# Kernel optimization log

Hardware: AMD Instinct MI355X
Metric: run time of the kernel (lower is better)

## Reference

```python
import jax, jax.numpy as jnp
import numpy as np

B, T, K = 16, 8, 4          # batch, num task vectors, num param blocks
DIN, H1, F, MH = 9408, 1024, 512, 128  # encoder dims; MetaNet hidden


def _pool(x):
    # 4x4 average pool then flatten: [B,3,224,224] -> [B, 3*56*56]
    b = x.shape[0]
    return x.reshape(b, 3, 56, 4, 56, 4).mean(axis=(3, 5)).reshape(b, -1)


def setup_inputs() -> dict:
    key = jax.random.key(0)
    ks = jax.random.split(key, 13)
    n = lambda k, shp, sc: jax.random.normal(k, shp, jnp.float32) * sc
    return {
        "x": jax.random.normal(ks[0], (B, 3, 224, 224), jnp.float32),
        "W1": n(ks[1], (DIN, H1), 0.02), "b1": n(ks[2], (H1,), 0.02),
        "W2": n(ks[3], (H1, F), 0.02),  "b2": n(ks[4], (F,), 0.02),
        "dW1": n(ks[5], (T, DIN, H1), 0.01), "db1": n(ks[6], (T, H1), 0.01),
        "dW2": n(ks[7], (T, H1, F), 0.01),   "db2": n(ks[8], (T, F), 0.01),
        # MetaNet: Linear(F,MH) init std=0.01, ReLU, Linear(MH, T*K)
        "mW1": n(ks[9], (F, MH), 0.01), "mb1": n(ks[10], (MH,), 0.01),
        "mW2": n(ks[11], (MH, T * K), 0.02), "mb2": n(ks[12], (T * K,), 0.02),
    }


def reference(x, W1, b1, W2, b2, dW1, db1, dW2, db2, mW1, mb1, mW2, mb2):
    xp = _pool(x)  # [B, DIN]
    # base features with frozen base params (torch.no_grad)
    base = jax.lax.stop_gradient(
        jax.nn.relu(xp @ W1 + b1) @ W2 + b2)  # [B, F]
    # MetaNet -> blockwise coefficients [B, T, K]; block order (W1,b1,W2,b2)
    coefs = (jax.nn.relu(base @ mW1 + mb1) @ mW2 + mb2).reshape(B, T, K)
    cW1, cb1, cW2, cb2 = coefs[:, :, 0], coefs[:, :, 1], coefs[:, :, 2], coefs[:, :, 3]
    # per-sample composed forward; (W1 + sum_t c*dW1) applied to xp, factored
    # so the [B,DIN,H1] composed weight is never materialized:
    h_tv = jnp.einsum("bi,tij->btj", xp, dW1)            # [B,T,H1]
    h = jax.nn.relu(xp @ W1 + jnp.einsum("bt,btj->bj", cW1, h_tv)
                    + b1 + jnp.einsum("bt,tj->bj", cb1, db1))  # [B,H1]
    o_tv = jnp.einsum("bj,tjk->btk", h, dW2)             # [B,T,F]
    out = (h @ W2 + jnp.einsum("bt,btk->bk", cW2, o_tv)
           + b2 + jnp.einsum("bt,tk->bk", cb2, db2))     # [B,F]
    return out
```

## Files before the change

### kernel.cpp

```cpp
#include <hip/hip_runtime.h>
#include <cstdint>
#include <cstddef>


typedef float f2_t __attribute__((ext_vector_type(2)));
typedef float f4_t __attribute__((ext_vector_type(4)));

template<int KC, int VEC, int UF, int NT>
__device__ __forceinline__ void gemm_pipe(
    const float* a_s, int row0, const float* Brow, int N, float (&acc)[16][VEC])
{
  static_assert(KC % UF == 0, "");
  constexpr int NG = KC / UF;
  static_assert(NG >= 2, "");
  float w0[UF][VEC], w1[UF][VEC];

  auto loadg = [&](float (&W)[UF][VEC], int kb) {
#pragma unroll
    for (int u = 0; u < UF; ++u) {
      const float* p = Brow + (size_t)(kb + u) * N;
      if constexpr (VEC == 2) {
        f2_t v;
        if constexpr (NT) v = __builtin_nontemporal_load(reinterpret_cast<const f2_t*>(p));
        else              v = *reinterpret_cast<const f2_t*>(p);
        W[u][0] = v.x; W[u][1] = v.y;
      } else {
        f4_t v;
        if constexpr (NT) v = __builtin_nontemporal_load(reinterpret_cast<const f4_t*>(p));
        else              v = *reinterpret_cast<const f4_t*>(p);
        W[u][0] = v.x; W[u][1] = v.y; W[u][2] = v.z; W[u][3] = v.w;
      }
    }
  };
  auto comp = [&](const float (&W)[UF][VEC], int kb) {
#pragma unroll
    for (int u = 0; u < UF; ++u) {
      int kk = row0 + kb + u;
      const float4 a0 = *reinterpret_cast<const float4*>(&a_s[kk * 20 + 0]);
      const float4 a1 = *reinterpret_cast<const float4*>(&a_s[kk * 20 + 4]);
      const float4 a2 = *reinterpret_cast<const float4*>(&a_s[kk * 20 + 8]);
      const float4 a3 = *reinterpret_cast<const float4*>(&a_s[kk * 20 + 12]);
      const float av[16] = {a0.x, a0.y, a0.z, a0.w, a1.x, a1.y, a1.z, a1.w,
                            a2.x, a2.y, a2.z, a2.w, a3.x, a3.y, a3.z, a3.w};
#pragma unroll
      for (int b = 0; b < 16; ++b)
#pragma unroll
        for (int v = 0; v < VEC; ++v)
          acc[b][v] = fmaf(av[b], W[u][v], acc[b][v]);
    }
  };

  loadg(w0, 0);
  if constexpr (NG % 2 == 0) {
#pragma unroll 1
    for (int g = 0; g + 2 < NG; g += 2) {
      loadg(w1, (g + 1) * UF);
      comp(w0, g * UF);
      loadg(w0, (g + 2) * UF);
      comp(w1, (g + 1) * UF);
    }
    loadg(w1, (NG - 1) * UF);
    comp(w0, (NG - 2) * UF);
    comp(w1, (NG - 1) * UF);
  } else {
#pragma unroll 1
    for (int g = 0; g + 3 < NG; g += 2) {
      loadg(w1, (g + 1) * UF);
      comp(w0, g * UF);
      loadg(w0, (g + 2) * UF);
      comp(w1, (g + 1) * UF);
    }
    loadg(w1, (NG - 2) * UF);
    comp(w0, (NG - 3) * UF);
    loadg(w0, (NG - 1) * UF);
    comp(w1, (NG - 2) * UF);
    comp(w0, (NG - 1) * UF);
  }
}

template<int KC, int NTHR>
__device__ __forceinline__ void stage_pool(float* a_s, const float* __restrict__ x, int il) {
  for (int idx = threadIdx.x; idx < 16 * KC; idx += NTHR) {
    int b = idx / KC, kk = idx - b * KC;
    int i = il + kk;
    int ch = i / 3136, r = i - ch * 3136;
    int pi = r / 56, pj = r - pi * 56;
    const float* src = x + ((size_t)(b * 3 + ch) * 224 + 4 * pi) * 224 + 4 * pj;
    float4 v0 = *reinterpret_cast<const float4*>(src);
    float4 v1 = *reinterpret_cast<const float4*>(src + 224);
    float4 v2 = *reinterpret_cast<const float4*>(src + 448);
    float4 v3 = *reinterpret_cast<const float4*>(src + 672);
    float s = (v0.x + v0.y + v0.z + v0.w) + (v1.x + v1.y + v1.z + v1.w)
            + (v2.x + v2.y + v2.z + v2.w) + (v3.x + v3.y + v3.z + v3.w);
    a_s[kk * 20 + b] = s * 0.0625f;
  }
}

__global__ __launch_bounds__(512, 2) void gbig_kernel(
    const float* __restrict__ x,
    const float* __restrict__ W1,
    const float* __restrict__ dW1,
    float* __restrict__ P1, float* __restrict__ P3)
{
  __shared__ float a_s[294 * 20];
  __shared__ float lds2[256 * 65];
  const int tid = threadIdx.x;

  if (blockIdx.x < 112) {
    const int c = blockIdx.x;
    stage_pool<84, 512>(a_s, x, c * 84);
    __syncthreads();

    const int j0 = tid * 2;
    float acc[16][2];
#pragma unroll
    for (int b = 0; b < 16; ++b) { acc[b][0] = 0.f; acc[b][1] = 0.f; }
    gemm_pipe<84, 2, 7, 1>(a_s, 0, W1 + (size_t)c * 84 * 1024 + j0, 1024, acc);

    float* Pb = P1 + (size_t)c * 16 * 1024 + j0;
#pragma unroll
    for (int b = 0; b < 16; ++b) {
      f2_t v = {acc[b][0], acc[b][1]};
      __builtin_nontemporal_store(v, reinterpret_cast<f2_t*>(Pb));
      Pb += 1024;
    }
  } else {
    const int c = blockIdx.x - 112;
    const int t = c >> 5, il = (c & 31) * 294;
    stage_pool<294, 512>(a_s, x, il);
    __syncthreads();

    const int half = tid >> 8, t256 = tid & 255;
    const int j0 = t256 * 4;
    float acc[16][4];
#pragma unroll
    for (int b = 0; b < 16; ++b)
#pragma unroll
      for (int v = 0; v < 4; ++v) acc[b][v] = 0.f;

    gemm_pipe<147, 4, 7, 1>(a_s, half * 147,
                            dW1 + ((size_t)t * 9408 + il + half * 147) * 1024 + j0,
                            1024, acc);

    if (half) {
      float* dst = &lds2[t256 * 65];
#pragma unroll
      for (int b = 0; b < 16; ++b)
#pragma unroll
        for (int v = 0; v < 4; ++v) dst[b * 4 + v] = acc[b][v];
    }
    __syncthreads();
    if (!half) {
      const float* src = &lds2[t256 * 65];
      float* Pb = P3 + (size_t)c * 16 * 1024 + j0;
#pragma unroll
      for (int b = 0; b < 16; ++b) {
        f4_t v = {acc[b][0] + src[b * 4 + 0], acc[b][1] + src[b * 4 + 1],
                  acc[b][2] + src[b * 4 + 2], acc[b][3] + src[b * 4 + 3]};
        __builtin_nontemporal_store(v, reinterpret_cast<f4_t*>(Pb));
        Pb += 1024;
      }
    }
  }
}

__global__ __launch_bounds__(256) void rg12_kernel(
    const float* __restrict__ P1, const float* __restrict__ b1,
    const float* __restrict__ W2,
    float* __restrict__ z1, float* __restrict__ P2)
{
  __shared__ float4 r[16][17];
  __shared__ float t1s[64];
  const int blk = blockIdx.x;
  const int b = blk >> 4, jg = blk & 15;
  const int fl = threadIdx.x & 15, s = threadIdx.x >> 4;
  const int f = blk * 64 + fl * 4;

  const f4_t* p = reinterpret_cast<const f4_t*>(P1 + (size_t)s * 7 * 16384 + f);
  float sx = 0.f, sy = 0.f, sz = 0.f, sw = 0.f;
#pragma unroll
  for (int cc = 0; cc < 7; ++cc) {
    f4_t v = __builtin_nontemporal_load(p);
    sx += v.x; sy += v.y; sz += v.z; sw += v.w;
    p += 4096;
  }
  r[s][fl] = make_float4(sx, sy, sz, sw);
  __syncthreads();

  if (s == 0) {
    float vx = 0.f, vy = 0.f, vz = 0.f, vw = 0.f;
#pragma unroll
    for (int i = 0; i < 16; ++i) {
      float4 t = r[i][fl];
      vx += t.x; vy += t.y; vz += t.z; vw += t.w;
    }
    float4 bb = *reinterpret_cast<const float4*>(b1 + (f & 1023));
    float4 z = make_float4(vx + bb.x, vy + bb.y, vz + bb.z, vw + bb.w);
    *reinterpret_cast<float4*>(z1 + f) = z;
    *reinterpret_cast<float4*>(&t1s[fl * 4]) =
        make_float4(fmaxf(z.x, 0.f), fmaxf(z.y, 0.f), fmaxf(z.z, 0.f), fmaxf(z.w, 0.f));
  }
  __syncthreads();

  const int j = threadIdx.x * 2;
  const float* w = W2 + (size_t)(jg * 64) * 512 + j;
  float a0 = 0.f, a1 = 0.f;
#pragma unroll 8
  for (int kk = 0; kk < 64; ++kk) {
    f2_t wv = *reinterpret_cast<const f2_t*>(w);
    w += 512;
    float tv = t1s[kk];
    a0 = fmaf(tv, wv.x, a0);
    a1 = fmaf(tv, wv.y, a1);
  }
  f2_t o = {a0, a1};
  __builtin_nontemporal_store(o, reinterpret_cast<f2_t*>(P2 + ((size_t)jg * 16 + b) * 512 + j));
}

template<int KC, int VEC, int UF, int NT, int BS>
__global__ __launch_bounds__(BS) void skinny_gemm(
    const float* __restrict__ A, int ldA,
    const float* __restrict__ B,
    const float* __restrict__ A2, int ldA2,
    const float* __restrict__ B2,
    int chunkSplit, int chunksPerT,
    const float* __restrict__ coefs4,
    int N, float* __restrict__ P)
{
  __shared__ float a_s[KC * 20];
  const int c = blockIdx.x, tid = threadIdx.x;

  const float* Ab;
  const float* Bb;
  int lda, iLoc0, t = 0;
  bool scaled = false;
  if (c < chunkSplit) {
    Ab = A; lda = ldA;
    if (chunksPerT > 0) {
      t = c / chunksPerT;
      iLoc0 = (c - t * chunksPerT) * KC;
    } else {
      iLoc0 = c * KC;
    }
    scaled = (coefs4 != nullptr);
    Bb = B + (size_t)c * KC * N;
  } else {
    Ab = A2; lda = ldA2;
    iLoc0 = (c - chunkSplit) * KC;
    Bb = B2 + (size_t)iLoc0 * N;
  }

  for (int b = 0; b < 16; ++b) {
    float s = scaled ? coefs4[b * 32 + t * 4] : 1.f;
    const float* Arow = Ab + (size_t)b * lda + iLoc0;
    for (int kk = tid; kk < KC; kk += BS)
      a_s[kk * 20 + b] = s * Arow[kk];
  }
  __syncthreads();

  const int j0 = (blockIdx.y * BS + tid) * VEC;
  float acc[16][VEC];
#pragma unroll
  for (int b = 0; b < 16; ++b)
#pragma unroll
    for (int v = 0; v < VEC; ++v) acc[b][v] = 0.f;

  gemm_pipe<KC, VEC, UF, NT>(a_s, 0, Bb + j0, N, acc);

  float* Pb = P + (size_t)c * 16 * N + j0;
#pragma unroll
  for (int b = 0; b < 16; ++b) {
    if constexpr (VEC == 2) {
      f2_t v = {acc[b][0], acc[b][1]};
      __builtin_nontemporal_store(v, reinterpret_cast<f2_t*>(Pb));
    } else {
      f4_t v = {acc[b][0], acc[b][1], acc[b][2], acc[b][3]};
      __builtin_nontemporal_store(v, reinterpret_cast<f4_t*>(Pb));
    }
    Pb += N;
  }
}

template<int NCH, int MODE, int FTOT>
__global__ __launch_bounds__(256) void reduce4(
    const float* __restrict__ P,
    const float* __restrict__ bias,
    const float* __restrict__ coefs,
    const float* __restrict__ dvec,
    float* __restrict__ o1)
{
  constexpr int CPS = NCH / 16;
  static_assert(NCH % 16 == 0, "");
  __shared__ float4 r[16][17];
  const int fl = threadIdx.x & 15, s = threadIdx.x >> 4;
  const int f = blockIdx.x * 64 + fl * 4;

  const f4_t* p = reinterpret_cast<const f4_t*>(P + (size_t)s * CPS * FTOT + f);
  float sx = 0.f, sy = 0.f, sz = 0.f, sw = 0.f;
#pragma unroll 8
  for (int cc = 0; cc < CPS; ++cc) {
    f4_t v = __builtin_nontemporal_load(p);
    sx += v.x; sy += v.y; sz += v.z; sw += v.w;
    p += FTOT / 4;
  }
  if constexpr (MODE == 3) {
    int b = f >> 10;
    float sc = coefs[b * 32 + (s >> 1) * 4];
    sx *= sc; sy *= sc; sz *= sc; sw *= sc;
  }
  r[s][fl] = make_float4(sx, sy, sz, sw);
  __syncthreads();

  if (s == 0) {
    float vx = 0.f, vy = 0.f, vz = 0.f, vw = 0.f;
#pragma unroll
    for (int i = 0; i < 16; ++i) {
      float4 t = r[i][fl];
      vx += t.x; vy += t.y; vz += t.z; vw += t.w;
    }
    if constexpr (MODE == 3) {
      int b = f >> 10, j = f & 1023;
      float4 zz = *reinterpret_cast<const float4*>(bias + f);
      float zx = vx + zz.x, zy = vy + zz.y, zzc = vz + zz.z, zw = vw + zz.w;
#pragma unroll
      for (int t = 0; t < 8; ++t) {
        float c1 = coefs[b * 32 + t * 4 + 1];
        float4 d = *reinterpret_cast<const float4*>(dvec + t * 1024 + j);
        zx = fmaf(c1, d.x, zx); zy = fmaf(c1, d.y, zy);
        zzc = fmaf(c1, d.z, zzc); zw = fmaf(c1, d.w, zw);
      }
      *reinterpret_cast<float4*>(o1 + f) =
          make_float4(fmaxf(zx, 0.f), fmaxf(zy, 0.f), fmaxf(zzc, 0.f), fmaxf(zw, 0.f));
    } else {
      int b = f >> 9, k = f & 511;
      float4 bb = *reinterpret_cast<const float4*>(bias + k);
      float zx = vx + bb.x, zy = vy + bb.y, zzc = vz + bb.z, zw = vw + bb.w;
#pragma unroll
      for (int t = 0; t < 8; ++t) {
        float c3 = coefs[b * 32 + t * 4 + 3];
        float4 d = *reinterpret_cast<const float4*>(dvec + t * 512 + k);
        zx = fmaf(c3, d.x, zx); zy = fmaf(c3, d.y, zy);
        zzc = fmaf(c3, d.z, zzc); zw = fmaf(c3, d.w, zw);
      }
      *reinterpret_cast<float4*>(o1 + f) = make_float4(zx, zy, zzc, zw);
    }
  }
}

__global__ __launch_bounds__(512) void tail2_kernel(
    const float* __restrict__ P2, const float* __restrict__ b2,
    const float* __restrict__ mW1, const float* __restrict__ mb1,
    const float* __restrict__ mW2, const float* __restrict__ mb2,
    float* __restrict__ coefs)
{
  __shared__ float bs[512];
  __shared__ float pm[4][129];
  __shared__ float ms[128];
  __shared__ float p3[16][33];
  const int b = blockIdx.x, tid = threadIdx.x;

  float s = b2[tid];
  const float* p = P2 + b * 512 + tid;
#pragma unroll
  for (int c = 0; c < 16; ++c) { s += *p; p += 8192; }
  bs[tid] = s;
  __syncthreads();

  {
    int col = tid & 127, kq = tid >> 7;
    const float* br = &bs[kq * 128];
    const float* w = mW1 + (size_t)(kq * 128) * 128 + col;
    float m0 = 0.f, m1 = 0.f, m2 = 0.f, m3 = 0.f;
    for (int k = 0; k < 128; k += 4) {
      m0 = fmaf(br[k + 0], w[(k + 0) * 128], m0);
      m1 = fmaf(br[k + 1], w[(k + 1) * 128], m1);
      m2 = fmaf(br[k + 2], w[(k + 2) * 128], m2);
      m3 = fmaf(br[k + 3], w[(k + 3) * 128], m3);
    }
    pm[kq][col] = (m0 + m1) + (m2 + m3);
  }
  __syncthreads();
  if (tid < 128)
    ms[tid] = fmaxf(mb1[tid] + (pm[0][tid] + pm[1][tid]) + (pm[2][tid] + pm[3][tid]), 0.f);
  __syncthreads();

  {
    int o = tid & 31, kq = tid >> 5;
    float a = 0.f;
#pragma unroll
    for (int kk = 0; kk < 8; ++kk)
      a = fmaf(ms[kq * 8 + kk], mW2[(kq * 8 + kk) * 32 + o], a);
    p3[kq][o] = a;
  }
  __syncthreads();
  if (tid < 32) {
    float a = mb2[tid];
#pragma unroll
    for (int q = 0; q < 16; ++q) a += p3[q][tid];
    coefs[b * 32 + tid] = a;
  }
}

extern "C" void kernel_launch(void* const* d_in, const int* in_sizes, int n_in,
                              void* d_out, int out_size, void* d_ws, size_t ws_size,
                              hipStream_t stream) {
  const float* x   = (const float*)d_in[0];
  const float* W1  = (const float*)d_in[1];
  const float* b1  = (const float*)d_in[2];
  const float* W2  = (const float*)d_in[3];
  const float* b2  = (const float*)d_in[4];
  const float* dW1 = (const float*)d_in[5];
  const float* db1 = (const float*)d_in[6];
  const float* dW2 = (const float*)d_in[7];
  const float* db2 = (const float*)d_in[8];
  const float* mW1 = (const float*)d_in[9];
  const float* mb1 = (const float*)d_in[10];
  const float* mW2 = (const float*)d_in[11];
  const float* mb2 = (const float*)d_in[12];
  float* out = (float*)d_out;

  float* ws    = (float*)d_ws;
  float* z1    = ws;
  float* coefs = z1 + 16384;
  float* h     = coefs + 512;
  float* P1    = h + 16384;
  float* P2    = P1 + 1835008;
  float* P3    = P2 + 131072;
  float* P4    = P3 + 4194304;

  gbig_kernel<<<368, 512, 0, stream>>>(x, W1, dW1, P1, P3);

  rg12_kernel<<<256, 256, 0, stream>>>(P1, b1, W2, z1, P2);

  tail2_kernel<<<16, 512, 0, stream>>>(P2, b2, mW1, mb1, mW2, mb2, coefs);

  reduce4<256, 3, 16384><<<256, 256, 0, stream>>>(P3, z1, coefs, db1, h);

  skinny_gemm<32, 2, 8, 1, 256><<<dim3(288, 1), 256, 0, stream>>>(
      h, 1024, dW2, h, 1024, W2, 256, 32, coefs + 2, 512, P4);

  reduce4<288, 4, 8192><<<128, 256, 0, stream>>>(P4, b2, coefs, db2, out);
}
```

Baseline: 133.1 us.

## Split pooling into its own kernel and retile big GEMM into 256-thread blocks

Average pooling moves out of the fused GEMM kernel into a separate pool kernel that writes xp to workspace. The dW1 work is split into 512 blocks of 147 rows each, with no in-block LDS reduction of two halves, and the W1 path widens to 4 columns per thread. This removes redundant per-block pooling of x and the LDS partial-sum exchange, and raises block count and occupancy. In exchange it adds a kernel launch and doubles the P3 partial buffer, so the reduce4 pass reads twice as many partials.

```diff
diff --git a/kernel.cpp b/kernel.cpp
--- a/kernel.cpp
+++ b/kernel.cpp
@@ -6,9 +6,25 @@
 typedef float f2_t __attribute__((ext_vector_type(2)));
 typedef float f4_t __attribute__((ext_vector_type(4)));
 
+__global__ void pool_kernel(const float* __restrict__ x, float* __restrict__ xp) {
+  int idx = blockIdx.x * 256 + threadIdx.x;
+  int bc = idx / 3136;
+  int r  = idx - bc * 3136;
+  int i  = r / 56;
+  int j  = r - i * 56;
+  const float* src = x + ((size_t)bc * 224 + 4 * i) * 224 + 4 * j;
+  float s = 0.f;
+#pragma unroll
+  for (int rr = 0; rr < 4; ++rr) {
+    float4 v = *reinterpret_cast<const float4*>(src + rr * 224);
+    s += v.x + v.y + v.z + v.w;
+  }
+  xp[idx] = s * 0.0625f;
+}
+
 template<int KC, int VEC, int UF, int NT>
 __device__ __forceinline__ void gemm_pipe(
-    const float* a_s, int row0, const float* Brow, int N, float (&acc)[16][VEC])
+    const float* a_s, const float* Brow, int N, float (&acc)[16][VEC])
 {
   static_assert(KC % UF == 0, "");
   constexpr int NG = KC / UF;
@@ -35,7 +51,7 @@
   auto comp = [&](const float (&W)[UF][VEC], int kb) {
 #pragma unroll
     for (int u = 0; u < UF; ++u) {
-      int kk = row0 + kb + u;
+      int kk = kb + u;
       const float4 a0 = *reinterpret_cast<const float4*>(&a_s[kk * 20 + 0]);
       const float4 a1 = *reinterpret_cast<const float4*>(&a_s[kk * 20 + 4]);
       const float4 a2 = *reinterpret_cast<const float4*>(&a_s[kk * 20 + 8]);
@@ -78,88 +94,63 @@
   }
 }
 
-template<int KC, int NTHR>
-__device__ __forceinline__ void stage_pool(float* a_s, const float* __restrict__ x, int il) {
-  for (int idx = threadIdx.x; idx < 16 * KC; idx += NTHR) {
-    int b = idx / KC, kk = idx - b * KC;
-    int i = il + kk;
-    int ch = i / 3136, r = i - ch * 3136;
-    int pi = r / 56, pj = r - pi * 56;
-    const float* src = x + ((size_t)(b * 3 + ch) * 224 + 4 * pi) * 224 + 4 * pj;
-    float4 v0 = *reinterpret_cast<const float4*>(src);
-    float4 v1 = *reinterpret_cast<const float4*>(src + 224);
-    float4 v2 = *reinterpret_cast<const float4*>(src + 448);
-    float4 v3 = *reinterpret_cast<const float4*>(src + 672);
-    float s = (v0.x + v0.y + v0.z + v0.w) + (v1.x + v1.y + v1.z + v1.w)
-            + (v2.x + v2.y + v2.z + v2.w) + (v3.x + v3.y + v3.z + v3.w);
-    a_s[kk * 20 + b] = s * 0.0625f;
-  }
-}
-
-__global__ __launch_bounds__(512, 2) void gbig_kernel(
-    const float* __restrict__ x,
+__global__ __launch_bounds__(256, 3) void gbig2_kernel(
+    const float* __restrict__ xp,
     const float* __restrict__ W1,
     const float* __restrict__ dW1,
     float* __restrict__ P1, float* __restrict__ P3)
 {
-  __shared__ float a_s[294 * 20];
-  __shared__ float lds2[256 * 65];
+  __shared__ float a_s[147 * 20];
   const int tid = threadIdx.x;
 
-  if (blockIdx.x < 112) {
+  if (blockIdx.x < 512) {
     const int c = blockIdx.x;
-    stage_pool<84, 512>(a_s, x, c * 84);
+    const int t = c >> 6, il = (c & 63) * 147;
+    for (int b = 0; b < 16; ++b) {
+      const float* Arow = xp + (size_t)b * 9408 + il;
+      for (int kk = tid; kk < 147; kk += 256) a_s[kk * 20 + b] = Arow[kk];
+    }
     __syncthreads();
 
-    const int j0 = tid * 2;
-    float acc[16][2];
-#pragma unroll
-    for (int b = 0; b < 16; ++b) { acc[b][0] = 0.f; acc[b][1] = 0.f; }
-    gemm_pipe<84, 2, 7, 1>(a_s, 0, W1 + (size_t)c * 84 * 1024 + j0, 1024, acc);
+    const int j0 = tid * 4;
+    float acc[16][4];
+#pragma unroll
+    for (int b = 0; b < 16; ++b)
+#pragma unroll
+      for (int v = 0; v < 4; ++v) acc[b][v] = 0.f;
+
+    gemm_pipe<147, 4, 7, 1>(a_s, dW1 + ((size_t)t * 9408 + il) * 1024 + j0, 1024, acc);
+
+    float* Pb = P3 + (size_t)c * 16 * 1024 + j0;
+#pragma unroll
+    for (int b = 0; b < 16; ++b) {
+      f4_t v = {acc[b][0], acc[b][1], acc[b][2], acc[b][3]};
+      __builtin_nontemporal_store(v, reinterpret_cast<f4_t*>(Pb));
+      Pb += 1024;
+    }
+  } else {
+    const int c = blockIdx.x - 512;
+    for (int b = 0; b < 16; ++b) {
+      const float* Arow = xp + (size_t)b * 9408 + c * 84;
+      for (int kk = tid; kk < 84; kk += 256) a_s[kk * 20 + b] = Arow[kk];
+    }
+    __syncthreads();
+
+    const int j0 = tid * 4;
+    float acc[16][4];
+#pragma unroll
+    for (int b = 0; b < 16; ++b)
+#pragma unroll
+      for (int v = 0; v < 4; ++v) acc[b][v] = 0.f;
+
+    gemm_pipe<84, 4, 7, 1>(a_s, W1 + (size_t)c * 84 * 1024 + j0, 1024, acc);
 
     float* Pb = P1 + (size_t)c * 16 * 1024 + j0;
 #pragma unroll
     for (int b = 0; b < 16; ++b) {
-      f2_t v = {acc[b][0], acc[b][1]};
-      __builtin_nontemporal_store(v, reinterpret_cast<f2_t*>(Pb));
+      f4_t v = {acc[b][0], acc[b][1], acc[b][2], acc[b][3]};
+      __builtin_nontemporal_store(v, reinterpret_cast<f4_t*>(Pb));
       Pb += 1024;
-    }
-  } else {
-    const int c = blockIdx.x - 112;
-    const int t = c >> 5, il = (c & 31) * 294;
-    stage_pool<294, 512>(a_s, x, il);
-    __syncthreads();
-
-    const int half = tid >> 8, t256 = tid & 255;
-    const int j0 = t256 * 4;
-    float acc[16][4];
-#pragma unroll
-    for (int b = 0; b < 16; ++b)
-#pragma unroll
-      for (int v = 0; v < 4; ++v) acc[b][v] = 0.f;
-
-    gemm_pipe<147, 4, 7, 1>(a_s, half * 147,
-                            dW1 + ((size_t)t * 9408 + il + half * 147) * 1024 + j0,
-                            1024, acc);
-
-    if (half) {
-      float* dst = &lds2[t256 * 65];
-#pragma unroll
-      for (int b = 0; b < 16; ++b)
-#pragma unroll
-        for (int v = 0; v < 4; ++v) dst[b * 4 + v] = acc[b][v];
-    }
-    __syncthreads();
-    if (!half) {
-      const float* src = &lds2[t256 * 65];
-      float* Pb = P3 + (size_t)c * 16 * 1024 + j0;
-#pragma unroll
-      for (int b = 0; b < 16; ++b) {
-        f4_t v = {acc[b][0] + src[b * 4 + 0], acc[b][1] + src[b * 4 + 1],
-                  acc[b][2] + src[b * 4 + 2], acc[b][3] + src[b * 4 + 3]};
-        __builtin_nontemporal_store(v, reinterpret_cast<f4_t*>(Pb));
-        Pb += 1024;
-      }
     }
   }
 }
@@ -265,7 +256,7 @@
 #pragma unroll
     for (int v = 0; v < VEC; ++v) acc[b][v] = 0.f;
 
-  gemm_pipe<KC, VEC, UF, NT>(a_s, 0, Bb + j0, N, acc);
+  gemm_pipe<KC, VEC, UF, NT>(a_s, Bb + j0, N, acc);
 
   float* Pb = P + (size_t)c * 16 * N + j0;
 #pragma unroll
@@ -420,21 +411,24 @@
   float* out = (float*)d_out;
 
   float* ws    = (float*)d_ws;
-  float* z1    = ws;
+  float* xp    = ws;
+  float* z1    = xp + 150528;
   float* coefs = z1 + 16384;
   float* h     = coefs + 512;
   float* P1    = h + 16384;
   float* P2    = P1 + 1835008;
   float* P3    = P2 + 131072;
-  float* P4    = P3 + 4194304;
-
-  gbig_kernel<<<368, 512, 0, stream>>>(x, W1, dW1, P1, P3);
+  float* P4    = P3 + 8388608;
+
+  pool_kernel<<<588, 256, 0, stream>>>(x, xp);
+
+  gbig2_kernel<<<624, 256, 0, stream>>>(xp, W1, dW1, P1, P3);
 
   rg12_kernel<<<256, 256, 0, stream>>>(P1, b1, W2, z1, P2);
 
   tail2_kernel<<<16, 512, 0, stream>>>(P2, b2, mW1, mb1, mW2, mb2, coefs);
 
-  reduce4<256, 3, 16384><<<256, 256, 0, stream>>>(P3, z1, coefs, db1, h);
+  reduce4<512, 3, 16384><<<256, 256, 0, stream>>>(P3, z1, coefs, db1, h);
 
   skinny_gemm<32, 2, 8, 1, 256><<<dim3(288, 1), 256, 0, stream>>>(
       h, 1024, dW2, h, 1024, W2, 256, 32, coefs + 2, 512, P4);
```

Measured after the change: 166.1 us. +24.8%, slower.
